# Kernel optimization log

Hardware: AMD Instinct MI355X
Metric: run time of the kernel (lower is better)

Reference implementation:

```python
import jax, jax.numpy as jnp
import numpy as np

N_NODES = 100000

def setup_inputs() -> dict:
    key = jax.random.key(0)
    k1, k2, k3, k4 = jax.random.split(key, 4)
    B, S, D, H = 50000, 10, 128, 128
    nodes = jax.random.randint(k1, (B,), 0, N_NODES, dtype=jnp.int64 if jax.config.jax_enable_x64 else jnp.int32)
    neigh_idx = jax.random.randint(k2, (B, S), 0, N_NODES, dtype=nodes.dtype)
    feature = jax.random.normal(k3, (N_NODES, D), dtype=jnp.float32)
    weight = jax.random.normal(k4, (2 * D, H), dtype=jnp.float32) * (1.0 / np.sqrt(2 * D))
    return {"nodes": nodes, "neigh_idx": neigh_idx, "feature": feature, "weight": weight}

def reference(nodes, neigh_idx, feature, weight):
    # Mean aggregation over sampled neighbors: [B, S, D] -> [B, D]
    neigh_feats = jnp.mean(feature[neigh_idx], axis=1)
    # Self features: [B, D]
    self_feats = feature[nodes]
    # Concat + linear + ReLU (gcn=False branch)
    combined = jnp.concatenate([self_feats, neigh_feats], axis=1)  # [B, 2D]
    return jax.nn.relu(combined @ weight)  # [B, H]
```

## Files before the change

kernel.cpp:

```cpp
#include <hip/hip_runtime.h>


typedef __attribute__((ext_vector_type(8))) short bf16x8;
typedef __attribute__((ext_vector_type(4))) float f32x4;

__device__ __forceinline__ unsigned short f2bf(float x) {
  unsigned int u = __float_as_uint(x);
  u += 0x7fffu + ((u >> 16) & 1u);
  return (unsigned short)(u >> 16);
}

__global__ void sage_prep_wt(const float* __restrict__ W,
                             unsigned short* __restrict__ Wt) {
  int tid = blockIdx.x * blockDim.x + threadIdx.x;
  const float4* W4 = (const float4*)W;
  float4 v = W4[tid];
  int flat = tid << 2;
  int k = flat >> 7;
  int h = flat & 127;
  Wt[(h + 0) * 256 + k] = f2bf(v.x);
  Wt[(h + 1) * 256 + k] = f2bf(v.y);
  Wt[(h + 2) * 256 + k] = f2bf(v.z);
  Wt[(h + 3) * 256 + k] = f2bf(v.w);
}

__global__ __launch_bounds__(256, 6)
void sage_gather(const int* __restrict__ nodes,
                 const int* __restrict__ neigh,
                 const float* __restrict__ feat,
                 unsigned short* __restrict__ comb,
                 int B)
{
  const int t   = threadIdx.x;
  const int r   = t >> 4;
  const int sub = t & 15;
  const int b   = blockIdx.x * 16 + r;
  if (b >= B) return;

  const float4* fbase = (const float4*)feat;
  const long srow = (long)nodes[b] * 32;
  float4 s0 = fbase[srow + sub];
  float4 s1 = fbase[srow + 16 + sub];

  float m0x=0.f,m0y=0.f,m0z=0.f,m0w=0.f, m1x=0.f,m1y=0.f,m1z=0.f,m1w=0.f;
#pragma unroll
  for (int s = 0; s < 10; ++s) {
    const long nrow = (long)neigh[b * 10 + s] * 32;
    float4 v0 = fbase[nrow + sub];
    float4 v1 = fbase[nrow + 16 + sub];
    m0x += v0.x; m0y += v0.y; m0z += v0.z; m0w += v0.w;
    m1x += v1.x; m1y += v1.y; m1z += v1.z; m1w += v1.w;
  }

  ushort4* crow = (ushort4*)(comb + (size_t)b * 256);
  ushort4 a, c;
  a.x = f2bf(s0.x); a.y = f2bf(s0.y); a.z = f2bf(s0.z); a.w = f2bf(s0.w);
  crow[sub] = a;
  a.x = f2bf(s1.x); a.y = f2bf(s1.y); a.z = f2bf(s1.z); a.w = f2bf(s1.w);
  crow[16 + sub] = a;
  c.x = f2bf(m0x * 0.1f); c.y = f2bf(m0y * 0.1f);
  c.z = f2bf(m0z * 0.1f); c.w = f2bf(m0w * 0.1f);
  crow[32 + sub] = c;
  c.x = f2bf(m1x * 0.1f); c.y = f2bf(m1y * 0.1f);
  c.z = f2bf(m1z * 0.1f); c.w = f2bf(m1w * 0.1f);
  crow[48 + sub] = c;
}

__global__ __launch_bounds__(512, 4)
void sage_gemm(const unsigned short* __restrict__ comb,
               const unsigned short* __restrict__ Wt,
               float* __restrict__ out,
               int B)
{
  constexpr int K = 256, H = 128, STR = K + 8;
  __shared__ unsigned short Clds[64 * STR];

  const int t = threadIdx.x;
  const int block0 = blockIdx.x * 64;

  const uint4* c4 = (const uint4*)comb;
#pragma unroll
  for (int p = 0; p < 4; ++p) {
    int c = p * 512 + t;
    int row = c >> 5;
    int off = (c & 31) * 8;
    int gb = block0 + row;
    uint4 v;
    if (gb < B) v = c4[(size_t)gb * 32 + (c & 31)];
    else { v.x = v.y = v.z = v.w = 0u; }
    *(uint4*)&Clds[row * STR + off] = v;
  }
  __syncthreads();

  const int lane = t & 63;
  const int wave = t >> 6;
  const int m    = lane & 15;
  const int quad = lane >> 4;
  const int cbase = wave * 16;

  bf16x8 bfrag[8];
#pragma unroll
  for (int ks = 0; ks < 8; ++ks)
    bfrag[ks] = *(const bf16x8*)&Wt[(cbase + m) * K + ks * 32 + quad * 8];

  f32x4 acc[4];
#pragma unroll
  for (int rt = 0; rt < 4; ++rt) acc[rt] = (f32x4){0.f, 0.f, 0.f, 0.f};

#pragma unroll
  for (int ks = 0; ks < 8; ++ks) {
    const int koff = ks * 32 + quad * 8;
#pragma unroll
    for (int rt = 0; rt < 4; ++rt) {
      bf16x8 a = *(const bf16x8*)&Clds[(rt * 16 + m) * STR + koff];
      acc[rt] = __builtin_amdgcn_mfma_f32_16x16x32_bf16(a, bfrag[ks], acc[rt], 0, 0, 0);
    }
  }

#pragma unroll
  for (int rt = 0; rt < 4; ++rt) {
#pragma unroll
    for (int reg = 0; reg < 4; ++reg) {
      const int row = rt * 16 + quad * 4 + reg;
      const int gb = block0 + row;
      if (gb < B) out[(size_t)gb * H + cbase + m] = fmaxf(acc[rt][reg], 0.0f);
    }
  }
}

extern "C" void kernel_launch(void* const* d_in, const int* in_sizes, int n_in,
                              void* d_out, int out_size, void* d_ws, size_t ws_size,
                              hipStream_t stream) {
  const int*   nodes = (const int*)d_in[0];
  const int*   neigh = (const int*)d_in[1];
  const float* feat  = (const float*)d_in[2];
  const float* W     = (const float*)d_in[3];
  float*       out   = (float*)d_out;
  const int B = in_sizes[0];

  unsigned short* Wt = (unsigned short*)d_ws;
  const size_t need = 65536 + (size_t)B * 256 * 2;
  unsigned short* comb = (ws_size >= need)
                           ? (unsigned short*)((char*)d_ws + 65536)
                           : (unsigned short*)d_out;

  sage_prep_wt<<<32, 256, 0, stream>>>(W, Wt);
  sage_gather<<<(B + 15) / 16, 256, 0, stream>>>(nodes, neigh, feat, comb, B);
  sage_gemm<<<(B + 63) / 64, 512, 0, stream>>>(comb, Wt, out, B);
}
```

Measured before the change: 142.1 us.

## Fuse gather into GEMM with bf16 feature table and swizzled LDS

The separate gather and GEMM kernels become one fused kernel that gathers self and mean-neighbor features straight into LDS, so the bf16 combined matrix is no longer written to and read back from global memory. When the workspace is large enough, a prep kernel first converts the whole feature table to bf16, which halves the bytes moved by the random gathers. The cost is an extra full pass over the 51 MB fp32 table on every call. The padded LDS stride is replaced by an XOR swizzle to avoid bank conflicts. Accumulating neighbors from bf16-rounded inputs also changes numerics slightly.

```diff
diff --git a/kernel.cpp b/kernel.cpp
--- a/kernel.cpp
+++ b/kernel.cpp
@@ -9,12 +9,16 @@
   u += 0x7fffu + ((u >> 16) & 1u);
   return (unsigned short)(u >> 16);
 }
+__device__ __forceinline__ unsigned int pack2bf(float lo, float hi) {
+  return (unsigned int)f2bf(lo) | ((unsigned int)f2bf(hi) << 16);
+}
+__device__ __forceinline__ float bflo(unsigned int u) { return __uint_as_float(u << 16); }
+__device__ __forceinline__ float bfhi(unsigned int u) { return __uint_as_float(u & 0xffff0000u); }
 
 __global__ void sage_prep_wt(const float* __restrict__ W,
                              unsigned short* __restrict__ Wt) {
   int tid = blockIdx.x * blockDim.x + threadIdx.x;
-  const float4* W4 = (const float4*)W;
-  float4 v = W4[tid];
+  float4 v = ((const float4*)W)[tid];
   int flat = tid << 2;
   int k = flat >> 7;
   int h = flat & 127;
@@ -24,71 +28,91 @@
   Wt[(h + 3) * 256 + k] = f2bf(v.w);
 }
 
-__global__ __launch_bounds__(256, 6)
-void sage_gather(const int* __restrict__ nodes,
-                 const int* __restrict__ neigh,
-                 const float* __restrict__ feat,
-                 unsigned short* __restrict__ comb,
-                 int B)
-{
-  const int t   = threadIdx.x;
-  const int r   = t >> 4;
-  const int sub = t & 15;
-  const int b   = blockIdx.x * 16 + r;
-  if (b >= B) return;
-
-  const float4* fbase = (const float4*)feat;
-  const long srow = (long)nodes[b] * 32;
-  float4 s0 = fbase[srow + sub];
-  float4 s1 = fbase[srow + 16 + sub];
-
-  float m0x=0.f,m0y=0.f,m0z=0.f,m0w=0.f, m1x=0.f,m1y=0.f,m1z=0.f,m1w=0.f;
-#pragma unroll
-  for (int s = 0; s < 10; ++s) {
-    const long nrow = (long)neigh[b * 10 + s] * 32;
-    float4 v0 = fbase[nrow + sub];
-    float4 v1 = fbase[nrow + 16 + sub];
-    m0x += v0.x; m0y += v0.y; m0z += v0.z; m0w += v0.w;
-    m1x += v1.x; m1y += v1.y; m1z += v1.z; m1w += v1.w;
-  }
-
-  ushort4* crow = (ushort4*)(comb + (size_t)b * 256);
-  ushort4 a, c;
-  a.x = f2bf(s0.x); a.y = f2bf(s0.y); a.z = f2bf(s0.z); a.w = f2bf(s0.w);
-  crow[sub] = a;
-  a.x = f2bf(s1.x); a.y = f2bf(s1.y); a.z = f2bf(s1.z); a.w = f2bf(s1.w);
-  crow[16 + sub] = a;
-  c.x = f2bf(m0x * 0.1f); c.y = f2bf(m0y * 0.1f);
-  c.z = f2bf(m0z * 0.1f); c.w = f2bf(m0w * 0.1f);
-  crow[32 + sub] = c;
-  c.x = f2bf(m1x * 0.1f); c.y = f2bf(m1y * 0.1f);
-  c.z = f2bf(m1z * 0.1f); c.w = f2bf(m1w * 0.1f);
-  crow[48 + sub] = c;
+__global__ void sage_prep_feat(const float* __restrict__ feat,
+                               unsigned int* __restrict__ fb, int n4) {
+  int tid = blockIdx.x * blockDim.x + threadIdx.x;
+  if (tid >= n4) return;
+  float4 v = ((const float4*)feat)[tid];
+  uint2 o; o.x = pack2bf(v.x, v.y); o.y = pack2bf(v.z, v.w);
+  ((uint2*)fb)[tid] = o;
 }
 
+template <bool BT>
 __global__ __launch_bounds__(512, 4)
-void sage_gemm(const unsigned short* __restrict__ comb,
-               const unsigned short* __restrict__ Wt,
-               float* __restrict__ out,
-               int B)
+void sage_fused2(const int* __restrict__ nodes,
+                 const int* __restrict__ neigh,
+                 const float* __restrict__ featf,
+                 const uint4* __restrict__ featb,
+                 const unsigned short* __restrict__ Wt,
+                 float* __restrict__ out, int B)
 {
-  constexpr int K = 256, H = 128, STR = K + 8;
-  __shared__ unsigned short Clds[64 * STR];
+  constexpr int K = 256, H = 128, S = 10;
+  __shared__ unsigned short Clds[64 * 256];
 
   const int t = threadIdx.x;
   const int block0 = blockIdx.x * 64;
 
-  const uint4* c4 = (const uint4*)comb;
+  {
+    const int r   = t >> 3;
+    const int sub = t & 7;
+    const int b   = block0 + r;
+    const int key = r & 7;
+    uint4* c0 = (uint4*)&Clds[r * 256 + ((sub     ) ^ key) * 8];
+    uint4* c1 = (uint4*)&Clds[r * 256 + ((sub +  8) ^ key) * 8];
+    uint4* c2 = (uint4*)&Clds[r * 256 + ((sub + 16) ^ key) * 8];
+    uint4* c3 = (uint4*)&Clds[r * 256 + ((sub + 24) ^ key) * 8];
+    if (b < B) {
+      float a0[8], a1[8];
 #pragma unroll
-  for (int p = 0; p < 4; ++p) {
-    int c = p * 512 + t;
-    int row = c >> 5;
-    int off = (c & 31) * 8;
-    int gb = block0 + row;
-    uint4 v;
-    if (gb < B) v = c4[(size_t)gb * 32 + (c & 31)];
-    else { v.x = v.y = v.z = v.w = 0u; }
-    *(uint4*)&Clds[row * STR + off] = v;
+      for (int i = 0; i < 8; ++i) { a0[i] = 0.f; a1[i] = 0.f; }
+      uint4 s0, s1;
+      if (BT) {
+        const long srow = (long)nodes[b] * 16;
+        s0 = featb[srow + sub];
+        s1 = featb[srow + 8 + sub];
+#pragma unroll
+        for (int s = 0; s < S; ++s) {
+          const long nrow = (long)neigh[b * S + s] * 16;
+          uint4 v0 = featb[nrow + sub];
+          uint4 v1 = featb[nrow + 8 + sub];
+          a0[0] += bflo(v0.x); a0[1] += bfhi(v0.x); a0[2] += bflo(v0.y); a0[3] += bfhi(v0.y);
+          a0[4] += bflo(v0.z); a0[5] += bfhi(v0.z); a0[6] += bflo(v0.w); a0[7] += bfhi(v0.w);
+          a1[0] += bflo(v1.x); a1[1] += bfhi(v1.x); a1[2] += bflo(v1.y); a1[3] += bfhi(v1.y);
+          a1[4] += bflo(v1.z); a1[5] += bfhi(v1.z); a1[6] += bflo(v1.w); a1[7] += bfhi(v1.w);
+        }
+      } else {
+        const float4* f4 = (const float4*)featf;
+        const long srow = (long)nodes[b] * 32;
+        float4 p, q;
+        p = f4[srow + 2 * sub]; q = f4[srow + 2 * sub + 1];
+        s0.x = pack2bf(p.x, p.y); s0.y = pack2bf(p.z, p.w);
+        s0.z = pack2bf(q.x, q.y); s0.w = pack2bf(q.z, q.w);
+        p = f4[srow + 16 + 2 * sub]; q = f4[srow + 17 + 2 * sub];
+        s1.x = pack2bf(p.x, p.y); s1.y = pack2bf(p.z, p.w);
+        s1.z = pack2bf(q.x, q.y); s1.w = pack2bf(q.z, q.w);
+#pragma unroll
+        for (int s = 0; s < S; ++s) {
+          const long nrow = (long)neigh[b * S + s] * 32;
+          float4 v;
+          v = f4[nrow + 2 * sub];      a0[0] += v.x; a0[1] += v.y; a0[2] += v.z; a0[3] += v.w;
+          v = f4[nrow + 2 * sub + 1];  a0[4] += v.x; a0[5] += v.y; a0[6] += v.z; a0[7] += v.w;
+          v = f4[nrow + 16 + 2 * sub]; a1[0] += v.x; a1[1] += v.y; a1[2] += v.z; a1[3] += v.w;
+          v = f4[nrow + 17 + 2 * sub]; a1[4] += v.x; a1[5] += v.y; a1[6] += v.z; a1[7] += v.w;
+        }
+      }
+      *c0 = s0;
+      *c1 = s1;
+      uint4 m0, m1;
+      m0.x = pack2bf(a0[0] * 0.1f, a0[1] * 0.1f); m0.y = pack2bf(a0[2] * 0.1f, a0[3] * 0.1f);
+      m0.z = pack2bf(a0[4] * 0.1f, a0[5] * 0.1f); m0.w = pack2bf(a0[6] * 0.1f, a0[7] * 0.1f);
+      m1.x = pack2bf(a1[0] * 0.1f, a1[1] * 0.1f); m1.y = pack2bf(a1[2] * 0.1f, a1[3] * 0.1f);
+      m1.z = pack2bf(a1[4] * 0.1f, a1[5] * 0.1f); m1.w = pack2bf(a1[6] * 0.1f, a1[7] * 0.1f);
+      *c2 = m0;
+      *c3 = m1;
+    } else {
+      uint4 z; z.x = z.y = z.z = z.w = 0u;
+      *c0 = z; *c1 = z; *c2 = z; *c3 = z;
+    }
   }
   __syncthreads();
 
@@ -97,6 +121,7 @@
   const int m    = lane & 15;
   const int quad = lane >> 4;
   const int cbase = wave * 16;
+  const int mk   = m & 7;
 
   bf16x8 bfrag[8];
 #pragma unroll
@@ -109,10 +134,10 @@
 
 #pragma unroll
   for (int ks = 0; ks < 8; ++ks) {
-    const int koff = ks * 32 + quad * 8;
+    const int pj = ((ks * 4 + quad) ^ mk) * 8;
 #pragma unroll
     for (int rt = 0; rt < 4; ++rt) {
-      bf16x8 a = *(const bf16x8*)&Clds[(rt * 16 + m) * STR + koff];
+      bf16x8 a = *(const bf16x8*)&Clds[(rt * 16 + m) * 256 + pj];
       acc[rt] = __builtin_amdgcn_mfma_f32_16x16x32_bf16(a, bfrag[ks], acc[rt], 0, 0, 0);
     }
   }
@@ -136,15 +161,23 @@
   const float* feat  = (const float*)d_in[2];
   const float* W     = (const float*)d_in[3];
   float*       out   = (float*)d_out;
-  const int B = in_sizes[0];
+  const int B  = in_sizes[0];
+  const int nf = in_sizes[2];
+  const int nf4 = nf / 4;
 
   unsigned short* Wt = (unsigned short*)d_ws;
-  const size_t need = 65536 + (size_t)B * 256 * 2;
-  unsigned short* comb = (ws_size >= need)
-                           ? (unsigned short*)((char*)d_ws + 65536)
-                           : (unsigned short*)d_out;
+  const size_t need = 65536 + (size_t)nf * 2;
 
   sage_prep_wt<<<32, 256, 0, stream>>>(W, Wt);
-  sage_gather<<<(B + 15) / 16, 256, 0, stream>>>(nodes, neigh, feat, comb, B);
-  sage_gemm<<<(B + 63) / 64, 512, 0, stream>>>(comb, Wt, out, B);
+  const int grid = (B + 63) / 64;
+
+  if (ws_size >= need) {
+    unsigned int* fb = (unsigned int*)((char*)d_ws + 65536);
+    sage_prep_feat<<<(nf4 + 255) / 256, 256, 0, stream>>>(feat, fb, nf4);
+    sage_fused2<true><<<grid, 512, 0, stream>>>(nodes, neigh, nullptr,
+                                                (const uint4*)fb, Wt, out, B);
+  } else {
+    sage_fused2<false><<<grid, 512, 0, stream>>>(nodes, neigh, feat,
+                                                 nullptr, Wt, out, B);
+  }
 }
```

Result: faster. 131.7 us (-7.3%).

## Fuse neighbor gather and bf16 GEMM into one kernel via LDS tile

Applied to the files above, without the earlier changes.

Merges the gather/mean kernel and the MFMA GEMM kernel into a single kernel. Each 512-thread block gathers 32 rows straight into LDS as bf16, then runs the matmul from LDS. This removes the global round-trip of the 25.6 MB combined buffer and one kernel launch. In exchange, each block reloads the weight fragments for only 32 rows, and the gather latency is no longer overlapped with other blocks' MFMA work except through occupancy.

```diff
diff --git a/kernel.cpp b/kernel.cpp
--- a/kernel.cpp
+++ b/kernel.cpp
@@ -13,8 +13,7 @@
 __global__ void sage_prep_wt(const float* __restrict__ W,
                              unsigned short* __restrict__ Wt) {
   int tid = blockIdx.x * blockDim.x + threadIdx.x;
-  const float4* W4 = (const float4*)W;
-  float4 v = W4[tid];
+  float4 v = ((const float4*)W)[tid];
   int flat = tid << 2;
   int k = flat >> 7;
   int h = flat & 127;
@@ -24,73 +23,63 @@
   Wt[(h + 3) * 256 + k] = f2bf(v.w);
 }
 
-__global__ __launch_bounds__(256, 6)
-void sage_gather(const int* __restrict__ nodes,
+__global__ __launch_bounds__(512, 6)
+void sage_fused3(const int* __restrict__ nodes,
                  const int* __restrict__ neigh,
                  const float* __restrict__ feat,
-                 unsigned short* __restrict__ comb,
-                 int B)
+                 const unsigned short* __restrict__ Wt,
+                 float* __restrict__ out, int B)
 {
-  const int t   = threadIdx.x;
-  const int r   = t >> 4;
-  const int sub = t & 15;
-  const int b   = blockIdx.x * 16 + r;
-  if (b >= B) return;
-
-  const float4* fbase = (const float4*)feat;
-  const long srow = (long)nodes[b] * 32;
-  float4 s0 = fbase[srow + sub];
-  float4 s1 = fbase[srow + 16 + sub];
-
-  float m0x=0.f,m0y=0.f,m0z=0.f,m0w=0.f, m1x=0.f,m1y=0.f,m1z=0.f,m1w=0.f;
-#pragma unroll
-  for (int s = 0; s < 10; ++s) {
-    const long nrow = (long)neigh[b * 10 + s] * 32;
-    float4 v0 = fbase[nrow + sub];
-    float4 v1 = fbase[nrow + 16 + sub];
-    m0x += v0.x; m0y += v0.y; m0z += v0.z; m0w += v0.w;
-    m1x += v1.x; m1y += v1.y; m1z += v1.z; m1w += v1.w;
-  }
-
-  ushort4* crow = (ushort4*)(comb + (size_t)b * 256);
-  ushort4 a, c;
-  a.x = f2bf(s0.x); a.y = f2bf(s0.y); a.z = f2bf(s0.z); a.w = f2bf(s0.w);
-  crow[sub] = a;
-  a.x = f2bf(s1.x); a.y = f2bf(s1.y); a.z = f2bf(s1.z); a.w = f2bf(s1.w);
-  crow[16 + sub] = a;
-  c.x = f2bf(m0x * 0.1f); c.y = f2bf(m0y * 0.1f);
-  c.z = f2bf(m0z * 0.1f); c.w = f2bf(m0w * 0.1f);
-  crow[32 + sub] = c;
-  c.x = f2bf(m1x * 0.1f); c.y = f2bf(m1y * 0.1f);
-  c.z = f2bf(m1z * 0.1f); c.w = f2bf(m1w * 0.1f);
-  crow[48 + sub] = c;
-}
-
-__global__ __launch_bounds__(512, 4)
-void sage_gemm(const unsigned short* __restrict__ comb,
-               const unsigned short* __restrict__ Wt,
-               float* __restrict__ out,
-               int B)
-{
-  constexpr int K = 256, H = 128, STR = K + 8;
-  __shared__ unsigned short Clds[64 * STR];
+  constexpr int K = 256, H = 128, S = 10;
+  constexpr int TILE = 32;
+  constexpr int STR = K + 8;
+  __shared__ unsigned short Clds[TILE * STR];
 
   const int t = threadIdx.x;
-  const int block0 = blockIdx.x * 64;
+  const int block0 = blockIdx.x * TILE;
 
-  const uint4* c4 = (const uint4*)comb;
+  {
+    const int r   = t >> 4;
+    const int sub = t & 15;
+    const int b   = block0 + r;
+    unsigned short* crow = &Clds[r * STR];
+    if (b < B) {
+      const float4* f4 = (const float4*)feat;
+      const long srow = (long)nodes[b] * 32;
+      float4 s0 = f4[srow + sub];
+      float4 s1 = f4[srow + 16 + sub];
+
+      float ax0=0.f, ay0=0.f, az0=0.f, aw0=0.f;
+      float ax1=0.f, ay1=0.f, az1=0.f, aw1=0.f;
 #pragma unroll
-  for (int p = 0; p < 4; ++p) {
-    int c = p * 512 + t;
-    int row = c >> 5;
-    int off = (c & 31) * 8;
-    int gb = block0 + row;
-    uint4 v;
-    if (gb < B) v = c4[(size_t)gb * 32 + (c & 31)];
-    else { v.x = v.y = v.z = v.w = 0u; }
-    *(uint4*)&Clds[row * STR + off] = v;
+      for (int s = 0; s < S; ++s) {
+        const long nrow = (long)neigh[b * S + s] * 32;
+        float4 v0 = f4[nrow + sub];
+        float4 v1 = f4[nrow + 16 + sub];
+        ax0 += v0.x; ay0 += v0.y; az0 += v0.z; aw0 += v0.w;
+        ax1 += v1.x; ay1 += v1.y; az1 += v1.z; aw1 += v1.w;
+      }
+      ushort4 o;
+      o.x = f2bf(s0.x); o.y = f2bf(s0.y); o.z = f2bf(s0.z); o.w = f2bf(s0.w);
+      *(ushort4*)&crow[4 * sub] = o;
+      o.x = f2bf(s1.x); o.y = f2bf(s1.y); o.z = f2bf(s1.z); o.w = f2bf(s1.w);
+      *(ushort4*)&crow[64 + 4 * sub] = o;
+      o.x = f2bf(ax0 * 0.1f); o.y = f2bf(ay0 * 0.1f);
+      o.z = f2bf(az0 * 0.1f); o.w = f2bf(aw0 * 0.1f);
+      *(ushort4*)&crow[128 + 4 * sub] = o;
+      o.x = f2bf(ax1 * 0.1f); o.y = f2bf(ay1 * 0.1f);
+      o.z = f2bf(az1 * 0.1f); o.w = f2bf(aw1 * 0.1f);
+      *(ushort4*)&crow[192 + 4 * sub] = o;
+    } else {
+      ushort4 z; z.x = z.y = z.z = z.w = 0;
+      *(ushort4*)&crow[4 * sub] = z;
+      *(ushort4*)&crow[64 + 4 * sub] = z;
+      *(ushort4*)&crow[128 + 4 * sub] = z;
+      *(ushort4*)&crow[192 + 4 * sub] = z;
+    }
   }
   __syncthreads();
+  __builtin_amdgcn_sched_barrier(0);
 
   const int lane = t & 63;
   const int wave = t >> 6;
@@ -103,28 +92,24 @@
   for (int ks = 0; ks < 8; ++ks)
     bfrag[ks] = *(const bf16x8*)&Wt[(cbase + m) * K + ks * 32 + quad * 8];
 
-  f32x4 acc[4];
-#pragma unroll
-  for (int rt = 0; rt < 4; ++rt) acc[rt] = (f32x4){0.f, 0.f, 0.f, 0.f};
-
+  f32x4 acc0 = {0.f, 0.f, 0.f, 0.f};
+  f32x4 acc1 = {0.f, 0.f, 0.f, 0.f};
 #pragma unroll
   for (int ks = 0; ks < 8; ++ks) {
     const int koff = ks * 32 + quad * 8;
-#pragma unroll
-    for (int rt = 0; rt < 4; ++rt) {
-      bf16x8 a = *(const bf16x8*)&Clds[(rt * 16 + m) * STR + koff];
-      acc[rt] = __builtin_amdgcn_mfma_f32_16x16x32_bf16(a, bfrag[ks], acc[rt], 0, 0, 0);
-    }
+    bf16x8 a0 = *(const bf16x8*)&Clds[(m     ) * STR + koff];
+    bf16x8 a1 = *(const bf16x8*)&Clds[(16 + m) * STR + koff];
+    acc0 = __builtin_amdgcn_mfma_f32_16x16x32_bf16(a0, bfrag[ks], acc0, 0, 0, 0);
+    acc1 = __builtin_amdgcn_mfma_f32_16x16x32_bf16(a1, bfrag[ks], acc1, 0, 0, 0);
   }
 
 #pragma unroll
-  for (int rt = 0; rt < 4; ++rt) {
-#pragma unroll
-    for (int reg = 0; reg < 4; ++reg) {
-      const int row = rt * 16 + quad * 4 + reg;
-      const int gb = block0 + row;
-      if (gb < B) out[(size_t)gb * H + cbase + m] = fmaxf(acc[rt][reg], 0.0f);
-    }
+  for (int reg = 0; reg < 4; ++reg) {
+    const int row0 = quad * 4 + reg;
+    const int gb0 = block0 + row0;
+    const int gb1 = gb0 + 16;
+    if (gb0 < B) out[(size_t)gb0 * H + cbase + m] = fmaxf(acc0[reg], 0.0f);
+    if (gb1 < B) out[(size_t)gb1 * H + cbase + m] = fmaxf(acc1[reg], 0.0f);
   }
 }
 
@@ -139,12 +124,7 @@
   const int B = in_sizes[0];
 
   unsigned short* Wt = (unsigned short*)d_ws;
-  const size_t need = 65536 + (size_t)B * 256 * 2;
-  unsigned short* comb = (ws_size >= need)
-                           ? (unsigned short*)((char*)d_ws + 65536)
-                           : (unsigned short*)d_out;
-
   sage_prep_wt<<<32, 256, 0, stream>>>(W, Wt);
-  sage_gather<<<(B + 15) / 16, 256, 0, stream>>>(nodes, neigh, feat, comb, B);
-  sage_gemm<<<(B + 63) / 64, 512, 0, stream>>>(comb, Wt, out, B);
+  const int grid = (B + 31) / 32;
+  sage_fused3<<<grid, 512, 0, stream>>>(nodes, neigh, feat, Wt, out, B);
 }
```

Measured after the change: 129.6 us. -8.8%, faster.
